# Optimization experiments

Hardware: AMD Instinct MI355X
Metric: run time of the kernel (lower is better)

## Reference

```python
import jax, jax.numpy as jnp
import numpy as np

N = 30000   # nodes
E = 600000  # edges (avg degree 20)
H = 128     # hidden_channels
L = 4       # num_layers
G = 64      # graphs in batch


def _init(key, shape, fan_in):
    return (jax.random.normal(key, shape, jnp.float32) / np.sqrt(fan_in)).astype(jnp.float32)


def setup_inputs() -> dict:
    key = jax.random.key(0)
    ks = jax.random.split(key, 24)
    x = jax.random.normal(ks[0], (N, 1), jnp.float32)
    pos = jax.random.normal(ks[1], (N, 3), jnp.float32)
    edge_index = jax.random.randint(ks[2], (2, E), 0, N, dtype=jnp.int32).astype(jnp.int64)
    batch = jnp.sort(jax.random.randint(ks[3], (N,), 0, G, dtype=jnp.int32)).astype(jnp.int64)

    emb_w = _init(ks[4], (1, H), 1)
    emb_b = jnp.zeros((H,), jnp.float32)

    # stacked per-layer params: msg MLP (2H+1 -> H -> H), node MLP (2H -> H -> H)
    msg_w1 = _init(ks[5], (L, 2 * H + 1, H), 2 * H + 1)
    msg_b1 = jnp.zeros((L, H), jnp.float32)
    msg_w2 = _init(ks[6], (L, H, H), H)
    msg_b2 = jnp.zeros((L, H), jnp.float32)
    node_w1 = _init(ks[7], (L, 2 * H, H), 2 * H)
    node_b1 = jnp.zeros((L, H), jnp.float32)
    node_w2 = _init(ks[8], (L, H, H), H)
    node_b2 = jnp.zeros((L, H), jnp.float32)

    out_w1 = _init(ks[9], (H, 32), H)
    out_b1 = jnp.zeros((32,), jnp.float32)
    out_w2 = _init(ks[10], (32, 1), 32)
    out_b2 = jnp.zeros((1,), jnp.float32)

    return {
        "x": x, "pos": pos, "edge_index": edge_index, "batch": batch,
        "emb_w": emb_w, "emb_b": emb_b,
        "msg_w1": msg_w1, "msg_b1": msg_b1, "msg_w2": msg_w2, "msg_b2": msg_b2,
        "node_w1": node_w1, "node_b1": node_b1, "node_w2": node_w2, "node_b2": node_b2,
        "out_w1": out_w1, "out_b1": out_b1, "out_w2": out_w2, "out_b2": out_b2,
    }


def reference(x, pos, edge_index, batch,
              emb_w, emb_b,
              msg_w1, msg_b1, msg_w2, msg_b2,
              node_w1, node_b1, node_w2, node_b2,
              out_w1, out_b1, out_w2, out_b2):
    row, col = edge_index[0], edge_index[1]  # row = source j, col = target i
    # edge scalar: squared distance (computed once, reused across layers)
    dist_sq = jnp.sum((pos[row] - pos[col]) ** 2, axis=-1, keepdims=True)  # [E,1]

    h = x @ emb_w + emb_b  # [N,H]
    for l in range(L):
        x_j = h[row]   # source features
        x_i = h[col]   # target features
        m = jnp.concatenate([x_i, x_j, dist_sq], axis=-1)           # [E, 2H+1]
        m = jax.nn.silu(m @ msg_w1[l] + msg_b1[l]) @ msg_w2[l] + msg_b2[l]  # [E,H]
        aggr = jax.ops.segment_sum(m, col, num_segments=N)          # scatter-add to targets
        nh = jnp.concatenate([h, aggr], axis=-1)                    # [N, 2H]
        h = jax.nn.silu(nh @ node_w1[l] + node_b1[l]) @ node_w2[l] + node_b2[l]
        # dropout omitted for deterministic reference (eval mode)

    g = jax.ops.segment_sum(h, batch, num_segments=G)               # global_add_pool [G,H]
    return jax.nn.silu(g @ out_w1 + out_b1) @ out_w2 + out_b2       # [G,1]
```

## Files before the change

### kernel.cpp

```cpp
#include <hip/hip_runtime.h>

typedef unsigned short u16;
typedef __bf16 bf16x8 __attribute__((ext_vector_type(8)));
typedef float f32x4 __attribute__((ext_vector_type(4)));

#define HN 128
#define TM 64
#define LTM 32
#define ASTRIDE 136

__device__ __forceinline__ u16 f2bf(float f) {
  union { float f; unsigned u; } v; v.f = f;
  unsigned r = v.u + 0x7fffu + ((v.u >> 16) & 1u);
  return (u16)(r >> 16);
}
__device__ __forceinline__ float bf2f(u16 v) {
  union { unsigned u; float f; } x; x.u = ((unsigned)v) << 16; return x.f;
}
__device__ __forceinline__ float bflo(unsigned v) {
  union { unsigned u; float f; } x; x.u = v << 16; return x.f;
}
__device__ __forceinline__ float bfhi(unsigned v) {
  union { unsigned u; float f; } x; x.u = v & 0xffff0000u; return x.f;
}
__device__ __forceinline__ float silu_f(float x) {
  float e = __builtin_amdgcn_exp2f(-1.442695041f * x);
  return x * __builtin_amdgcn_rcpf(1.f + e);
}

__global__ void pack_weights(const float* __restrict__ msg_w1, const float* __restrict__ msg_w2,
                             const float* __restrict__ node_w1, const float* __restrict__ node_w2,
                             u16* __restrict__ pw, int* __restrict__ deg,
                             float* __restrict__ g, int N_, int GH) {
  int id = blockIdx.x * 256 + threadIdx.x;
  if (id < N_) deg[id] = 0;
  if (id < GH) g[id] = 0.f;
  if (id >= 4 * 6 * 16384) return;
  int l = id / (6 * 16384);
  int rem = id % (6 * 16384);
  int m = rem / 16384;
  int e = rem % 16384;
  int kg = e >> 10;
  int n = (e >> 3) & 127;
  int j = e & 7;
  int k = kg * 8 + j;
  float v = 0.f;
  switch (m) {
    case 0: v = msg_w1[(l * 257 + k) * 128 + n]; break;
    case 1: v = msg_w1[(l * 257 + 128 + k) * 128 + n]; break;
    case 2: v = msg_w2[(l * 128 + k) * 128 + n]; break;
    case 3: v = node_w1[(l * 256 + k) * 128 + n]; break;
    case 4: v = node_w1[(l * 256 + 128 + k) * 128 + n]; break;
    case 5: v = node_w2[(l * 128 + k) * 128 + n]; break;
  }
  pw[id] = f2bf(v);
}

__device__ __forceinline__ void gemm64(const u16* s_A, const u16* s_W,
                                       int w, int quad, int m16, f32x4 acc[8]) {
#pragma unroll
  for (int ks = 0; ks < 4; ks++) {
    bf16x8 a = *(const bf16x8*)&s_A[(w * 16 + m16) * ASTRIDE + ks * 32 + quad * 8];
#pragma unroll
    for (int ct = 0; ct < 8; ct++) {
      bf16x8 b = *(const bf16x8*)&s_W[(ks * 4 + quad) * 1024 + (ct * 16 + m16) * 8];
      acc[ct] = __builtin_amdgcn_mfma_f32_16x16x32_bf16(a, b, acc[ct], 0, 0, 0);
    }
  }
}

__device__ __forceinline__ void gemm32_gb(const u16* s_A, const u16* __restrict__ gW,
                                          int rh, int ch, int quad, int m16, f32x4 acc[4]) {
#pragma unroll
  for (int ks = 0; ks < 4; ks++) {
    bf16x8 a = *(const bf16x8*)&s_A[(rh * 16 + m16) * ASTRIDE + ks * 32 + quad * 8];
#pragma unroll
    for (int ct = 0; ct < 4; ct++) {
      bf16x8 b = *(const bf16x8*)&gW[(ks * 4 + quad) * 1024 + ((ch * 4 + ct) * 16 + m16) * 8];
      acc[ct] = __builtin_amdgcn_mfma_f32_16x16x32_bf16(a, b, acc[ct], 0, 0, 0);
    }
  }
}

__device__ __forceinline__ void gemm32_ra_gb(const bf16x8 aH[4], const u16* __restrict__ gW,
                                             int ch, int quad, int m16, f32x4 acc[4]) {
#pragma unroll
  for (int ks = 0; ks < 4; ks++) {
#pragma unroll
    for (int ct = 0; ct < 4; ct++) {
      bf16x8 b = *(const bf16x8*)&gW[(ks * 4 + quad) * 1024 + ((ch * 4 + ct) * 16 + m16) * 8];
      acc[ct] = __builtin_amdgcn_mfma_f32_16x16x32_bf16(aH[ks], b, acc[ct], 0, 0, 0);
    }
  }
}

__global__ __launch_bounds__(256) void fold_kernel(
    const float* __restrict__ msg_w2, const float* __restrict__ node_w1,
    const float* __restrict__ msg_b2, const u16* __restrict__ pw,
    u16* __restrict__ pwc, float* __restrict__ vc) {
  __shared__ __align__(16) u16 s_A[TM * ASTRIDE];
  __shared__ __align__(16) u16 s_W[16384];
  const int t = threadIdx.x;
  const int w = t >> 6, lane = t & 63, quad = lane >> 4, m16 = lane & 15;
  const int b = blockIdx.x, l = b >> 1, half = b & 1;
  const int tile0 = half * 64;

  {
    int r = t >> 2, qo = (t & 3) * 32;
    const float4* src = (const float4*)(msg_w2 + (size_t)(l * 128 + tile0 + r) * 128 + qo);
    u16* dst = s_A + r * ASTRIDE + qo;
#pragma unroll
    for (int i = 0; i < 8; i++) {
      float4 v = src[i];
      ushort4 o;
      o.x = f2bf(v.x); o.y = f2bf(v.y); o.z = f2bf(v.z); o.w = f2bf(v.w);
      *(ushort4*)(dst + i * 4) = o;
    }
  }
  {
    const int4* src = (const int4*)(pw + (size_t)(l * 6 + 4) * 16384);
    int4* dst = (int4*)s_W;
#pragma unroll
    for (int i = 0; i < 8; i++) dst[t + i * 256] = src[t + i * 256];
  }
  __syncthreads();
  f32x4 acc[8];
#pragma unroll
  for (int ct = 0; ct < 8; ct++) acc[ct] = {0.f, 0.f, 0.f, 0.f};
  gemm64(s_A, s_W, w, quad, m16, acc);
#pragma unroll
  for (int ct = 0; ct < 8; ct++)
#pragma unroll
    for (int j = 0; j < 4; j++) {
      int k = tile0 + w * 16 + quad * 4 + j;
      int n = ct * 16 + m16;
      pwc[(size_t)l * 16384 + (k >> 3) * 1024 + n * 8 + (k & 7)] = f2bf(acc[ct][j]);
    }
  if (half == 0 && t < 128) {
    float s = 0.f;
    for (int np = 0; np < 128; np++)
      s += msg_b2[l * 128 + np] * node_w1[(size_t)(l * 256 + 128 + np) * 128 + t];
    vc[l * 128 + t] = s;
  }
}

__global__ void hist_kernel(const int* __restrict__ eidx, int* __restrict__ deg,
                            int* __restrict__ rnk, int E_) {
  int e = blockIdx.x * 256 + threadIdx.x;
  if (e < E_) rnk[e] = atomicAdd(&deg[eidx[E_ + e]], 1);
}

__global__ void scan1_kernel(const int* __restrict__ deg, int* __restrict__ off,
                             int* __restrict__ bsum, int n) {
  __shared__ int s[256];
  int t = threadIdx.x;
  int i = blockIdx.x * 256 + t;
  int v = (i < n) ? deg[i] : 0;
  s[t] = v;
  for (int d = 1; d < 256; d <<= 1) {
    __syncthreads();
    int x = (t >= d) ? s[t - d] : 0;
    __syncthreads();
    s[t] += x;
  }
  __syncthreads();
  if (i < n) off[i] = s[t] - v;
  if (t == 255) bsum[blockIdx.x] = s[255];
}

__global__ void scan2_kernel(int* __restrict__ bsum, int nb) {
  __shared__ int s[256];
  int t = threadIdx.x;
  int v = (t < nb) ? bsum[t] : 0;
  s[t] = v;
  for (int d = 1; d < 256; d <<= 1) {
    __syncthreads();
    int x = (t >= d) ? s[t - d] : 0;
    __syncthreads();
    s[t] += x;
  }
  __syncthreads();
  if (t < nb) bsum[t] = s[t] - v;
}

__global__ void scan3_kernel(int* __restrict__ off, const int* __restrict__ bsum, int n) {
  int i = blockIdx.x * 256 + threadIdx.x;
  if (i < n) off[i] += bsum[blockIdx.x];
}

__global__ void scatter_kernel(const int* __restrict__ eidx, const float* __restrict__ pos,
                               const int* __restrict__ off, const int* __restrict__ rnk,
                               int2* __restrict__ es8, int E_) {
  int e = blockIdx.x * 256 + threadIdx.x;
  if (e >= E_) return;
  int sr = eidx[e], tg = eidx[E_ + e];
  float dx = pos[sr * 3 + 0] - pos[tg * 3 + 0];
  float dy = pos[sr * 3 + 1] - pos[tg * 3 + 1];
  float dz = pos[sr * 3 + 2] - pos[tg * 3 + 2];
  float d = dx * dx + dy * dy + dz * dz;
  int p = off[tg] + rnk[e];
  int2 v;
  v.x = sr | (tg << 15);
  v.y = __float_as_int(d);
  es8[p] = v;
}

__global__ __launch_bounds__(256) void proj_kernel(
    const float* __restrict__ x, const float* __restrict__ emb_w,
    const float* __restrict__ emb_b, u16* __restrict__ hbf,
    u16* __restrict__ Pout, u16* __restrict__ Qout,
    const u16* __restrict__ pw, const float* __restrict__ b1, int nnodes) {
  __shared__ __align__(16) u16 s_A[TM * ASTRIDE];
  __shared__ __align__(16) u16 s_W[16384];
  const int t = threadIdx.x;
  const int w = t >> 6, lane = t & 63, quad = lane >> 4, m16 = lane & 15;
  const int tile0 = blockIdx.x * TM;
  {
    int r = t >> 2, qo = (t & 3) * 32;
    int node = tile0 + r;
    if (node >= nnodes) node = nnodes - 1;
    float xv = x[node];
    u16 hv[32];
#pragma unroll
    for (int i = 0; i < 32; i++) hv[i] = f2bf(xv * emb_w[qo + i] + emb_b[qo + i]);
    u16* dst = s_A + r * ASTRIDE + qo;
#pragma unroll
    for (int i = 0; i < 4; i++) *(int4*)(dst + i * 8) = *(int4*)(hv + i * 8);
    u16* gd = hbf + (size_t)node * HN + qo;
#pragma unroll
    for (int i = 0; i < 4; i++) *(int4*)(gd + i * 8) = *(int4*)(hv + i * 8);
  }
  {
    const int4* src = (const int4*)pw;
    int4* dst = (int4*)s_W;
#pragma unroll
    for (int i = 0; i < 8; i++) dst[t + i * 256] = src[t + i * 256];
  }
  __syncthreads();
  f32x4 acc[8];
#pragma unroll
  for (int ct = 0; ct < 8; ct++) acc[ct] = {0.f, 0.f, 0.f, 0.f};
  gemm64(s_A, s_W, w, quad, m16, acc);
  __syncthreads();
  {
    const int4* src = (const int4*)(pw + 16384);
    int4* dst = (int4*)s_W;
#pragma unroll
    for (int i = 0; i < 8; i++) dst[t + i * 256] = src[t + i * 256];
  }
  float bb[8];
#pragma unroll
  for (int ct = 0; ct < 8; ct++) bb[ct] = b1[ct * 16 + m16];
#pragma unroll
  for (int ct = 0; ct < 8; ct++)
#pragma unroll
    for (int j = 0; j < 4; j++) {
      int n = tile0 + w * 16 + quad * 4 + j;
      if (n < nnodes) Pout[(size_t)n * HN + ct * 16 + m16] = f2bf(acc[ct][j] + bb[ct]);
    }
  __syncthreads();
#pragma unroll
  for (int ct = 0; ct < 8; ct++) acc[ct] = {0.f, 0.f, 0.f, 0.f};
  gemm64(s_A, s_W, w, quad, m16, acc);
#pragma unroll
  for (int ct = 0; ct < 8; ct++)
#pragma unroll
    for (int j = 0; j < 4; j++) {
      int n = tile0 + w * 16 + quad * 4 + j;
      if (n < nnodes) Qout[(size_t)n * HN + ct * 16 + m16] = f2bf(acc[ct][j]);
    }
}

__device__ __forceinline__ void edge_step_lds(
    int tg_s, float dd_s, unsigned qv,
    int& cur_s, float& p0, float& p1, float& s0, float& s1,
    const u16* __restrict__ P, float* s_S, int cp,
    float wd0, float wd1, int tile0) {
  if (tg_s != cur_s) {
    if (cur_s >= 0) {
      float* dst = &s_S[(cur_s - tile0) * HN + cp];
      atomicAdd(dst, s0);
      atomicAdd(dst + 1, s1);
    }
    cur_s = tg_s; s0 = 0.f; s1 = 0.f;
    int cg = tg_s < 0 ? 0 : tg_s;
    unsigned pv = *(const unsigned*)&P[(size_t)cg * HN + cp];
    p0 = bflo(pv); p1 = bfhi(pv);
  }
  float x0 = p0 + bflo(qv) + dd_s * wd0;
  float x1 = p1 + bfhi(qv) + dd_s * wd1;
  s0 += silu_f(x0);
  s1 += silu_f(x1);
}

template <bool FUSE>
__global__ __launch_bounds__(256) void layer_kernel(
    const u16* __restrict__ P, const u16* __restrict__ Q,
    const u16* __restrict__ hbf, u16* __restrict__ hout,
    const int* __restrict__ off, const int* __restrict__ deg,
    const float* __restrict__ w1d, const int2* __restrict__ es8,
    const u16* __restrict__ pwc, const float* __restrict__ vc,
    const u16* __restrict__ pwn, const float* __restrict__ b1, const float* __restrict__ b2,
    const u16* __restrict__ pw_next, const float* __restrict__ b1_next,
    u16* __restrict__ Pout, u16* __restrict__ Qout, int nnodes, int E_) {
  __shared__ float s_S[LTM * HN];
  __shared__ __align__(16) u16 s_A[LTM * ASTRIDE];
  const int t = threadIdx.x;
  const int w = t >> 6, lane = t & 63, quad = lane >> 4, m16 = lane & 15;
  const int tile0 = blockIdx.x * LTM;
  const int rh = w >> 1;
  const int ch = w & 1;

  {
    float4 z = {0.f, 0.f, 0.f, 0.f};
    float4* p4 = (float4*)s_S;
#pragma unroll
    for (int i = 0; i < 4; i++) p4[t + i * 256] = z;
  }
  __syncthreads();

  const int cp = lane * 2;
  const float2 wdv = *(const float2*)&w1d[cp];
  const float wd0 = wdv.x, wd1 = wdv.y;
  const int e_lo = off[tile0];
  const int e_hi = (tile0 + LTM < nnodes) ? off[tile0 + LTM] : E_;
  const int span = e_hi - e_lo;
  const int wstart = e_lo + (span * w) / 4;
  const int wend = e_lo + (span * (w + 1)) / 4;
  const int total = wend - wstart;
  const int nchunks = (total + 63) >> 6;

  int cur_s = -1;
  float s0 = 0.f, s1 = 0.f, p0 = 0.f, p1 = 0.f;

  if (nchunks > 0) {
    int2* ebuf = (int2*)(s_A + (w * 8) * ASTRIDE);
    {
      int e = wstart + lane;
      int2 v;
      if (e < wend) v = es8[e];
      else { v.x = (int)0xFFFF8000; v.y = 0; }
      ebuf[lane] = v;
    }
    asm volatile("s_waitcnt lgkmcnt(0)" ::: "memory");
    int tg[8]; float dd[8]; unsigned qv[8];
#pragma unroll
    for (int j = 0; j < 8; j++) {
      int2 v = ebuf[j];
      tg[j] = v.x >> 15; dd[j] = __int_as_float(v.y);
      qv[j] = *(const unsigned*)&Q[(size_t)(v.x & 0x7fff) * HN + cp];
    }

    for (int ci = 0; ci < nchunks; ci++) {
      const int2* cb = ebuf + (ci & 1) * 64;
      const int2* nb = ebuf + ((ci + 1) & 1) * 64;
      int2 vnext; vnext.x = (int)0xFFFF8000; vnext.y = 0;
      {
        int e = wstart + (ci + 1) * 64 + lane;
        if (ci + 1 < nchunks && e < wend) vnext = es8[e];
      }
#pragma unroll
      for (int g = 0; g < 7; g++) {
        int tgn[8]; float ddn[8]; unsigned qvn[8];
#pragma unroll
        for (int j = 0; j < 8; j++) {
          int2 v = cb[(g + 1) * 8 + j];
          tgn[j] = v.x >> 15; ddn[j] = __int_as_float(v.y);
          qvn[j] = *(const unsigned*)&Q[(size_t)(v.x & 0x7fff) * HN + cp];
        }
#pragma unroll
        for (int j = 0; j < 8; j++) {
          int tg_s = __builtin_amdgcn_readfirstlane(tg[j]);
          edge_step_lds(tg_s, dd[j], qv[j], cur_s, p0, p1, s0, s1, P, s_S, cp, wd0, wd1, tile0);
        }
#pragma unroll
        for (int j = 0; j < 8; j++) { tg[j] = tgn[j]; dd[j] = ddn[j]; qv[j] = qvn[j]; }
      }
      ebuf[((ci + 1) & 1) * 64 + lane] = vnext;
      asm volatile("s_waitcnt lgkmcnt(0)" ::: "memory");
      {
        int tgn[8]; float ddn[8]; unsigned qvn[8];
#pragma unroll
        for (int j = 0; j < 8; j++) {
          int2 v = nb[j];
          tgn[j] = v.x >> 15; ddn[j] = __int_as_float(v.y);
          qvn[j] = *(const unsigned*)&Q[(size_t)(v.x & 0x7fff) * HN + cp];
        }
#pragma unroll
        for (int j = 0; j < 8; j++) {
          int tg_s = __builtin_amdgcn_readfirstlane(tg[j]);
          edge_step_lds(tg_s, dd[j], qv[j], cur_s, p0, p1, s0, s1, P, s_S, cp, wd0, wd1, tile0);
        }
#pragma unroll
        for (int j = 0; j < 8; j++) { tg[j] = tgn[j]; dd[j] = ddn[j]; qv[j] = qvn[j]; }
      }
    }
    if (cur_s >= 0) {
      float* dst = &s_S[(cur_s - tile0) * HN + cp];
      atomicAdd(dst, s0);
      atomicAdd(dst + 1, s1);
    }
  }
  __syncthreads();

  {
    int srow = w * 8 + (lane >> 3);
    int scol = (lane & 7) * 16;
    const float4* src = (const float4*)&s_S[srow * HN + scol];
    u16* dst = s_A + srow * ASTRIDE + scol;
#pragma unroll
    for (int i = 0; i < 4; i++) {
      float4 v = src[i];
      ushort4 o;
      o.x = f2bf(v.x); o.y = f2bf(v.y); o.z = f2bf(v.z); o.w = f2bf(v.w);
      *(ushort4*)(dst + i * 4) = o;
    }
  }
  __syncthreads();

  float bb1[4], vcr[4], bb2[4], bbn[4];
#pragma unroll
  for (int ct = 0; ct < 4; ct++) {
    int c = (ch * 4 + ct) * 16 + m16;
    bb1[ct] = b1[c];
    vcr[ct] = vc[c];
    bb2[ct] = b2[c];
    bbn[ct] = FUSE ? b1_next[c] : 0.f;
  }
  int nodem = tile0 + rh * 16 + m16;
  if (nodem >= nnodes) nodem = nnodes - 1;

  f32x4 acc[4];
#pragma unroll
  for (int ct = 0; ct < 4; ct++) acc[ct] = {0.f, 0.f, 0.f, 0.f};
  gemm32_gb(s_A, pwc, rh, ch, quad, m16, acc);

  bf16x8 aH[4];
#pragma unroll
  for (int ks = 0; ks < 4; ks++)
    aH[ks] = *(const bf16x8*)&hbf[(size_t)nodem * HN + ks * 32 + quad * 8];
  gemm32_ra_gb(aH, pwn, ch, quad, m16, acc);

  {
    float degv[4];
#pragma unroll
    for (int j = 0; j < 4; j++) {
      int n = tile0 + rh * 16 + quad * 4 + j;
      if (n >= nnodes) n = nnodes - 1;
      degv[j] = (float)deg[n];
    }
#pragma unroll
    for (int ct = 0; ct < 4; ct++)
#pragma unroll
      for (int j = 0; j < 4; j++) {
        int row = rh * 16 + quad * 4 + j;
        float xv = acc[ct][j] + bb1[ct] + degv[j] * vcr[ct];
        s_A[row * ASTRIDE + (ch * 4 + ct) * 16 + m16] = f2bf(silu_f(xv));
      }
  }
  __syncthreads();

#pragma unroll
  for (int ct = 0; ct < 4; ct++) acc[ct] = {0.f, 0.f, 0.f, 0.f};
  gemm32_gb(s_A, pwn + 32768, rh, ch, quad, m16, acc);

#pragma unroll
  for (int ct = 0; ct < 4; ct++)
#pragma unroll
    for (int j = 0; j < 4; j++) {
      int row = rh * 16 + quad * 4 + j;
      int n = tile0 + row;
      u16 hv = f2bf(acc[ct][j] + bb2[ct]);
      if (n < nnodes) hout[(size_t)n * HN + (ch * 4 + ct) * 16 + m16] = hv;
      if (FUSE) s_A[row * ASTRIDE + (ch * 4 + ct) * 16 + m16] = hv;
    }

  if (FUSE) {
    __syncthreads();
#pragma unroll
    for (int ct = 0; ct < 4; ct++) acc[ct] = {0.f, 0.f, 0.f, 0.f};
    gemm32_gb(s_A, pw_next, rh, ch, quad, m16, acc);
#pragma unroll
    for (int ct = 0; ct < 4; ct++)
#pragma unroll
      for (int j = 0; j < 4; j++) {
        int n = tile0 + rh * 16 + quad * 4 + j;
        if (n < nnodes) Pout[(size_t)n * HN + (ch * 4 + ct) * 16 + m16] = f2bf(acc[ct][j] + bbn[ct]);
      }
#pragma unroll
    for (int ct = 0; ct < 4; ct++) acc[ct] = {0.f, 0.f, 0.f, 0.f};
    gemm32_gb(s_A, pw_next + 16384, rh, ch, quad, m16, acc);
#pragma unroll
    for (int ct = 0; ct < 4; ct++)
#pragma unroll
      for (int j = 0; j < 4; j++) {
        int n = tile0 + rh * 16 + quad * 4 + j;
        if (n < nnodes) Qout[(size_t)n * HN + (ch * 4 + ct) * 16 + m16] = f2bf(acc[ct][j]);
      }
  }
}

__global__ __launch_bounds__(256) void pool_kernel(
    const u16* __restrict__ h, const int* __restrict__ batch,
    float* __restrict__ g, int N) {
  __shared__ int s_b[64];
  const int t = threadIdx.x;
  const int n0 = blockIdx.x * 64;
  if (t < 64) {
    int n = n0 + t;
    s_b[t] = (n < N) ? batch[n] : -1;
  }
  __syncthreads();
  const int cp = (t & 63) * 2;
  const int rg = t >> 6;
  int cur = -1;
  float s0 = 0.f, s1 = 0.f;
#pragma unroll 4
  for (int i = 0; i < 16; i++) {
    int r = rg * 16 + i;
    int b = s_b[r];
    if (b < 0) break;
    if (b != cur) {
      if (cur >= 0) {
        atomicAdd(&g[cur * HN + cp], s0);
        atomicAdd(&g[cur * HN + cp + 1], s1);
      }
      cur = b; s0 = 0.f; s1 = 0.f;
    }
    unsigned v = *(const unsigned*)&h[(size_t)(n0 + r) * HN + cp];
    s0 += bf2f((u16)(v & 0xffffu));
    s1 += bf2f((u16)(v >> 16));
  }
  if (cur >= 0) {
    atomicAdd(&g[cur * HN + cp], s0);
    atomicAdd(&g[cur * HN + cp + 1], s1);
  }
}

__global__ __launch_bounds__(64) void out_kernel(
    const float* __restrict__ g, const float* __restrict__ w1,
    const float* __restrict__ b1, const float* __restrict__ w2,
    const float* __restrict__ b2, float* __restrict__ out) {
  const int gi = blockIdx.x;
  const int t = threadIdx.x;
  const int c = t & 31, kh = t >> 5;
  float s = 0.f;
  for (int k = kh * 64; k < kh * 64 + 64; k++)
    s += g[gi * HN + k] * w1[k * 32 + c];
  s += __shfl_down(s, 32);
  float r = 0.f;
  if (kh == 0) r = silu_f(s + b1[c]) * w2[c];
  r += __shfl_down(r, 16);
  r += __shfl_down(r, 8);
  r += __shfl_down(r, 4);
  r += __shfl_down(r, 2);
  r += __shfl_down(r, 1);
  if (t == 0) out[gi] = r + b2[0];
}

extern "C" void kernel_launch(void* const* d_in, const int* in_sizes, int n_in,
                              void* d_out, int out_size, void* d_ws, size_t ws_size,
                              hipStream_t stream) {
  const float* x = (const float*)d_in[0];
  const float* pos = (const float*)d_in[1];
  const int* eidx = (const int*)d_in[2];
  const int* batch = (const int*)d_in[3];
  const float* emb_w = (const float*)d_in[4];
  const float* emb_b = (const float*)d_in[5];
  const float* msg_w1 = (const float*)d_in[6];
  const float* msg_b1 = (const float*)d_in[7];
  const float* msg_w2 = (const float*)d_in[8];
  const float* msg_b2 = (const float*)d_in[9];
  const float* node_w1 = (const float*)d_in[10];
  const float* node_b1 = (const float*)d_in[11];
  const float* node_w2 = (const float*)d_in[12];
  const float* node_b2 = (const float*)d_in[13];
  const float* out_w1 = (const float*)d_in[14];
  const float* out_b1 = (const float*)d_in[15];
  const float* out_w2 = (const float*)d_in[16];
  const float* out_b2 = (const float*)d_in[17];
  float* outp = (float*)d_out;

  const int N = 30000, E = 600000, G = 64;
  const size_t NH = (size_t)N * HN;

  u16* hA = (u16*)d_ws;
  u16* hB = hA + NH;
  u16* Pa = hB + NH;
  u16* Qa = Pa + NH;
  u16* Pb = Qa + NH;
  u16* Qb = Pb + NH;
  int2* es8 = (int2*)(Qb + NH);
  int* deg = (int*)(es8 + E);
  int* off = deg + N;
  int* bsum = off + N;
  float* g = (float*)(bsum + 128);
  u16* pw = (u16*)(g + G * HN);
  u16* pwc = pw + (size_t)4 * 6 * 16384;
  float* vcb = (float*)(pwc + (size_t)4 * 16384);
  int* rnk = (int*)Pb;

  const int NB = (N + 255) / 256;
  const int NTB = (N + TM - 1) / TM;
  const int NLB = (N + LTM - 1) / LTM;

  pack_weights<<<(4 * 6 * 16384 + 255) / 256, 256, 0, stream>>>(
      msg_w1, msg_w2, node_w1, node_w2, pw, deg, g, N, G * HN);
  fold_kernel<<<8, 256, 0, stream>>>(msg_w2, node_w1, msg_b2, pw, pwc, vcb);

  hist_kernel<<<(E + 255) / 256, 256, 0, stream>>>(eidx, deg, rnk, E);
  scan1_kernel<<<NB, 256, 0, stream>>>(deg, off, bsum, N);
  scan2_kernel<<<1, 256, 0, stream>>>(bsum, NB);
  scan3_kernel<<<NB, 256, 0, stream>>>(off, bsum, N);
  scatter_kernel<<<(E + 255) / 256, 256, 0, stream>>>(eidx, pos, off, rnk, es8, E);

  proj_kernel<<<NTB, 256, 0, stream>>>(x, emb_w, emb_b, hA, Pa, Qa, pw, msg_b1, N);

  u16* hcur = hA;
  u16* hnext = hB;
  u16* Pin = Pa; u16* Qin = Qa;
  u16* Pot = Pb; u16* Qot = Qb;
  for (int l = 0; l < 4; l++) {
    const u16* pwl = pw + (size_t)(l * 6) * 16384;
    const float* w1d = msg_w1 + (size_t)(l * 257 + 256) * 128;
    if (l < 3) {
      const u16* pw_next = pw + (size_t)((l + 1) * 6) * 16384;
      layer_kernel<true><<<NLB, 256, 0, stream>>>(
          Pin, Qin, hcur, hnext, off, deg, w1d, es8,
          pwc + (size_t)l * 16384, vcb + l * 128,
          pwl + 3 * 16384, node_b1 + l * 128, node_b2 + l * 128,
          pw_next, msg_b1 + (l + 1) * 128, Pot, Qot, N, E);
    } else {
      layer_kernel<false><<<NLB, 256, 0, stream>>>(
          Pin, Qin, hcur, hnext, off, deg, w1d, es8,
          pwc + (size_t)l * 16384, vcb + l * 128,
          pwl + 3 * 16384, node_b1 + l * 128, node_b2 + l * 128,
          nullptr, nullptr, nullptr, nullptr, N, E);
    }
    u16* tmp = hcur; hcur = hnext; hnext = tmp;
    tmp = Pin; Pin = Pot; Pot = tmp;
    tmp = Qin; Qin = Qot; Qot = tmp;
  }

  pool_kernel<<<(N + 63) / 64, 256, 0, stream>>>(hcur, batch, g, N);
  out_kernel<<<G, 64, 0, stream>>>(g, out_w1, out_b1, out_w2, out_b2, outp);
}
```

Before: 399.4 us.

## Exploit rank-1 embedding to drop proj kernel and layer-0 gathers

Since h0 = x*emb_w + emb_b is rank-1 in x, the layer-0 message pre-activations become x_i*uP + vP + x_j*uQ, with the u/v vectors precomputed in fold_kernel. The proj_kernel that materialized h0, P and Q for all nodes is removed. Layer 0 now gathers one float of x per edge instead of a bf16 Q row slice, and rebuilds h0 on the fly for the node MLP. This removes one GEMM kernel launch plus large N×H reads and writes. The cost is a third template variant and slightly different rounding, since P and Q are no longer quantized to bf16.

```diff
diff --git a/kernel.cpp b/kernel.cpp
--- a/kernel.cpp
+++ b/kernel.cpp
@@ -97,7 +97,10 @@
 __global__ __launch_bounds__(256) void fold_kernel(
     const float* __restrict__ msg_w2, const float* __restrict__ node_w1,
     const float* __restrict__ msg_b2, const u16* __restrict__ pw,
-    u16* __restrict__ pwc, float* __restrict__ vc) {
+    u16* __restrict__ pwc, float* __restrict__ vc,
+    const float* __restrict__ msg_w1, const float* __restrict__ emb_w,
+    const float* __restrict__ emb_b, const float* __restrict__ msg_b1,
+    float* __restrict__ uv) {
   __shared__ __align__(16) u16 s_A[TM * ASTRIDE];
   __shared__ __align__(16) u16 s_W[16384];
   const int t = threadIdx.x;
@@ -141,6 +144,20 @@
     for (int np = 0; np < 128; np++)
       s += msg_b2[l * 128 + np] * node_w1[(size_t)(l * 256 + 128 + np) * 128 + t];
     vc[l * 128 + t] = s;
+  }
+  if (l == 0 && half == 1 && t < 128) {
+    float up = 0.f, vp = 0.f, uq = 0.f, vq = 0.f;
+    for (int k = 0; k < 128; k++) {
+      float wa = msg_w1[(size_t)k * 128 + t];
+      float wb = msg_w1[(size_t)(128 + k) * 128 + t];
+      up = fmaf(emb_w[k], wa, up);
+      vp = fmaf(emb_b[k], wa, vp);
+      uq = fmaf(emb_w[k], wb, uq);
+      vq = fmaf(emb_b[k], wb, vq);
+    }
+    uv[t] = up;
+    uv[128 + t] = vp + vq + msg_b1[t];
+    uv[256 + t] = uq;
   }
 }
 
@@ -205,72 +222,6 @@
   es8[p] = v;
 }
 
-__global__ __launch_bounds__(256) void proj_kernel(
-    const float* __restrict__ x, const float* __restrict__ emb_w,
-    const float* __restrict__ emb_b, u16* __restrict__ hbf,
-    u16* __restrict__ Pout, u16* __restrict__ Qout,
-    const u16* __restrict__ pw, const float* __restrict__ b1, int nnodes) {
-  __shared__ __align__(16) u16 s_A[TM * ASTRIDE];
-  __shared__ __align__(16) u16 s_W[16384];
-  const int t = threadIdx.x;
-  const int w = t >> 6, lane = t & 63, quad = lane >> 4, m16 = lane & 15;
-  const int tile0 = blockIdx.x * TM;
-  {
-    int r = t >> 2, qo = (t & 3) * 32;
-    int node = tile0 + r;
-    if (node >= nnodes) node = nnodes - 1;
-    float xv = x[node];
-    u16 hv[32];
-#pragma unroll
-    for (int i = 0; i < 32; i++) hv[i] = f2bf(xv * emb_w[qo + i] + emb_b[qo + i]);
-    u16* dst = s_A + r * ASTRIDE + qo;
-#pragma unroll
-    for (int i = 0; i < 4; i++) *(int4*)(dst + i * 8) = *(int4*)(hv + i * 8);
-    u16* gd = hbf + (size_t)node * HN + qo;
-#pragma unroll
-    for (int i = 0; i < 4; i++) *(int4*)(gd + i * 8) = *(int4*)(hv + i * 8);
-  }
-  {
-    const int4* src = (const int4*)pw;
-    int4* dst = (int4*)s_W;
-#pragma unroll
-    for (int i = 0; i < 8; i++) dst[t + i * 256] = src[t + i * 256];
-  }
-  __syncthreads();
-  f32x4 acc[8];
-#pragma unroll
-  for (int ct = 0; ct < 8; ct++) acc[ct] = {0.f, 0.f, 0.f, 0.f};
-  gemm64(s_A, s_W, w, quad, m16, acc);
-  __syncthreads();
-  {
-    const int4* src = (const int4*)(pw + 16384);
-    int4* dst = (int4*)s_W;
-#pragma unroll
-    for (int i = 0; i < 8; i++) dst[t + i * 256] = src[t + i * 256];
-  }
-  float bb[8];
-#pragma unroll
-  for (int ct = 0; ct < 8; ct++) bb[ct] = b1[ct * 16 + m16];
-#pragma unroll
-  for (int ct = 0; ct < 8; ct++)
-#pragma unroll
-    for (int j = 0; j < 4; j++) {
-      int n = tile0 + w * 16 + quad * 4 + j;
-      if (n < nnodes) Pout[(size_t)n * HN + ct * 16 + m16] = f2bf(acc[ct][j] + bb[ct]);
-    }
-  __syncthreads();
-#pragma unroll
-  for (int ct = 0; ct < 8; ct++) acc[ct] = {0.f, 0.f, 0.f, 0.f};
-  gemm64(s_A, s_W, w, quad, m16, acc);
-#pragma unroll
-  for (int ct = 0; ct < 8; ct++)
-#pragma unroll
-    for (int j = 0; j < 4; j++) {
-      int n = tile0 + w * 16 + quad * 4 + j;
-      if (n < nnodes) Qout[(size_t)n * HN + ct * 16 + m16] = f2bf(acc[ct][j]);
-    }
-}
-
 __device__ __forceinline__ void edge_step_lds(
     int tg_s, float dd_s, unsigned qv,
     int& cur_s, float& p0, float& p1, float& s0, float& s1,
@@ -293,7 +244,31 @@
   s1 += silu_f(x1);
 }
 
-template <bool FUSE>
+__device__ __forceinline__ void edge_step_r1(
+    int tg_s, float dd_s, float xs,
+    int& cur_s, float& p0, float& p1, float& s0, float& s1,
+    const float* s_xt, float* s_S, int cp,
+    float wd0, float wd1, float uP0, float uP1, float vP0, float vP1,
+    float uQ0, float uQ1, int tile0) {
+  if (tg_s != cur_s) {
+    if (cur_s >= 0) {
+      float* dst = &s_S[(cur_s - tile0) * HN + cp];
+      atomicAdd(dst, s0);
+      atomicAdd(dst + 1, s1);
+    }
+    cur_s = tg_s; s0 = 0.f; s1 = 0.f;
+    int ci = tg_s < 0 ? 0 : (tg_s - tile0);
+    float xt = s_xt[ci];
+    p0 = fmaf(xt, uP0, vP0);
+    p1 = fmaf(xt, uP1, vP1);
+  }
+  float x0 = fmaf(dd_s, wd0, fmaf(xs, uQ0, p0));
+  float x1 = fmaf(dd_s, wd1, fmaf(xs, uQ1, p1));
+  s0 += silu_f(x0);
+  s1 += silu_f(x1);
+}
+
+template <bool FUSE, bool RANK1>
 __global__ __launch_bounds__(256) void layer_kernel(
     const u16* __restrict__ P, const u16* __restrict__ Q,
     const u16* __restrict__ hbf, u16* __restrict__ hout,
@@ -302,9 +277,13 @@
     const u16* __restrict__ pwc, const float* __restrict__ vc,
     const u16* __restrict__ pwn, const float* __restrict__ b1, const float* __restrict__ b2,
     const u16* __restrict__ pw_next, const float* __restrict__ b1_next,
-    u16* __restrict__ Pout, u16* __restrict__ Qout, int nnodes, int E_) {
+    u16* __restrict__ Pout, u16* __restrict__ Qout,
+    const float* __restrict__ xin, const float* __restrict__ uv,
+    const float* __restrict__ emb_w, const float* __restrict__ emb_b,
+    int nnodes, int E_) {
   __shared__ float s_S[LTM * HN];
   __shared__ __align__(16) u16 s_A[LTM * ASTRIDE];
+  __shared__ float s_xt[LTM];
   const int t = threadIdx.x;
   const int w = t >> 6, lane = t & 63, quad = lane >> 4, m16 = lane & 15;
   const int tile0 = blockIdx.x * LTM;
@@ -316,6 +295,12 @@
     float4* p4 = (float4*)s_S;
 #pragma unroll
     for (int i = 0; i < 4; i++) p4[t + i * 256] = z;
+  }
+  if constexpr (RANK1) {
+    if (t < LTM) {
+      int n = tile0 + t;
+      s_xt[t] = (n < nnodes) ? xin[n] : 0.f;
+    }
   }
   __syncthreads();
 
@@ -333,72 +318,175 @@
   int cur_s = -1;
   float s0 = 0.f, s1 = 0.f, p0 = 0.f, p1 = 0.f;
 
-  if (nchunks > 0) {
-    int2* ebuf = (int2*)(s_A + (w * 8) * ASTRIDE);
-    {
-      int e = wstart + lane;
-      int2 v;
-      if (e < wend) v = es8[e];
-      else { v.x = (int)0xFFFF8000; v.y = 0; }
-      ebuf[lane] = v;
-    }
-    asm volatile("s_waitcnt lgkmcnt(0)" ::: "memory");
-    int tg[8]; float dd[8]; unsigned qv[8];
-#pragma unroll
-    for (int j = 0; j < 8; j++) {
-      int2 v = ebuf[j];
-      tg[j] = v.x >> 15; dd[j] = __int_as_float(v.y);
-      qv[j] = *(const unsigned*)&Q[(size_t)(v.x & 0x7fff) * HN + cp];
-    }
-
-    for (int ci = 0; ci < nchunks; ci++) {
-      const int2* cb = ebuf + (ci & 1) * 64;
-      const int2* nb = ebuf + ((ci + 1) & 1) * 64;
-      int2 vnext; vnext.x = (int)0xFFFF8000; vnext.y = 0;
+  if constexpr (RANK1) {
+    __shared__ float s_xs[4][2][64];
+    const float uP0 = uv[cp], uP1 = uv[cp + 1];
+    const float vP0 = uv[128 + cp], vP1 = uv[128 + cp + 1];
+    const float uQ0 = uv[256 + cp], uQ1 = uv[256 + cp + 1];
+    if (nchunks > 0) {
+      int2* ebuf = (int2*)(s_A + (w * 8) * ASTRIDE);
+      float* xsb = &s_xs[w][0][0];
       {
-        int e = wstart + (ci + 1) * 64 + lane;
-        if (ci + 1 < nchunks && e < wend) vnext = es8[e];
-      }
-#pragma unroll
-      for (int g = 0; g < 7; g++) {
-        int tgn[8]; float ddn[8]; unsigned qvn[8];
-#pragma unroll
-        for (int j = 0; j < 8; j++) {
-          int2 v = cb[(g + 1) * 8 + j];
-          tgn[j] = v.x >> 15; ddn[j] = __int_as_float(v.y);
-          qvn[j] = *(const unsigned*)&Q[(size_t)(v.x & 0x7fff) * HN + cp];
+        int e = wstart + lane;
+        int2 v;
+        if (e < wend) v = es8[e];
+        else { v.x = (int)0xFFFF8000; v.y = 0; }
+        float xl = xin[v.x & 0x7fff];
+        ebuf[lane] = v;
+        xsb[lane] = xl;
+      }
+      asm volatile("s_waitcnt lgkmcnt(0)" ::: "memory");
+      int tg[8]; float dd[8]; float xs[8];
+#pragma unroll
+      for (int j = 0; j < 8; j++) {
+        int2 v = ebuf[j];
+        tg[j] = v.x >> 15; dd[j] = __int_as_float(v.y);
+        xs[j] = xsb[j];
+      }
+
+      for (int ci = 0; ci < nchunks; ci++) {
+        const int cs = (ci & 1), ns = ((ci + 1) & 1);
+        const int2* cb = ebuf + cs * 64;
+        const float* cx = xsb + cs * 64;
+        const int2* nb = ebuf + ns * 64;
+        const float* nx = xsb + ns * 64;
+        int2 vnext; vnext.x = (int)0xFFFF8000; vnext.y = 0;
+        {
+          int e = wstart + (ci + 1) * 64 + lane;
+          if (ci + 1 < nchunks && e < wend) vnext = es8[e];
         }
 #pragma unroll
-        for (int j = 0; j < 8; j++) {
-          int tg_s = __builtin_amdgcn_readfirstlane(tg[j]);
-          edge_step_lds(tg_s, dd[j], qv[j], cur_s, p0, p1, s0, s1, P, s_S, cp, wd0, wd1, tile0);
+        for (int g = 0; g < 3; g++) {
+          int tgn[8]; float ddn[8]; float xsn[8];
+#pragma unroll
+          for (int j = 0; j < 8; j++) {
+            int2 v = cb[(g + 1) * 8 + j];
+            tgn[j] = v.x >> 15; ddn[j] = __int_as_float(v.y);
+            xsn[j] = cx[(g + 1) * 8 + j];
+          }
+#pragma unroll
+          for (int j = 0; j < 8; j++) {
+            int tg_s = __builtin_amdgcn_readfirstlane(tg[j]);
+            edge_step_r1(tg_s, dd[j], xs[j], cur_s, p0, p1, s0, s1, s_xt, s_S, cp,
+                         wd0, wd1, uP0, uP1, vP0, vP1, uQ0, uQ1, tile0);
+          }
+#pragma unroll
+          for (int j = 0; j < 8; j++) { tg[j] = tgn[j]; dd[j] = ddn[j]; xs[j] = xsn[j]; }
         }
-#pragma unroll
-        for (int j = 0; j < 8; j++) { tg[j] = tgn[j]; dd[j] = ddn[j]; qv[j] = qvn[j]; }
-      }
-      ebuf[((ci + 1) & 1) * 64 + lane] = vnext;
+        float xnext = xin[vnext.x & 0x7fff];
+#pragma unroll
+        for (int g = 3; g < 7; g++) {
+          int tgn[8]; float ddn[8]; float xsn[8];
+#pragma unroll
+          for (int j = 0; j < 8; j++) {
+            int2 v = cb[(g + 1) * 8 + j];
+            tgn[j] = v.x >> 15; ddn[j] = __int_as_float(v.y);
+            xsn[j] = cx[(g + 1) * 8 + j];
+          }
+#pragma unroll
+          for (int j = 0; j < 8; j++) {
+            int tg_s = __builtin_amdgcn_readfirstlane(tg[j]);
+            edge_step_r1(tg_s, dd[j], xs[j], cur_s, p0, p1, s0, s1, s_xt, s_S, cp,
+                         wd0, wd1, uP0, uP1, vP0, vP1, uQ0, uQ1, tile0);
+          }
+#pragma unroll
+          for (int j = 0; j < 8; j++) { tg[j] = tgn[j]; dd[j] = ddn[j]; xs[j] = xsn[j]; }
+        }
+        ebuf[ns * 64 + lane] = vnext;
+        xsb[ns * 64 + lane] = xnext;
+        asm volatile("s_waitcnt lgkmcnt(0)" ::: "memory");
+        {
+          int tgn[8]; float ddn[8]; float xsn[8];
+#pragma unroll
+          for (int j = 0; j < 8; j++) {
+            int2 v = nb[j];
+            tgn[j] = v.x >> 15; ddn[j] = __int_as_float(v.y);
+            xsn[j] = nx[j];
+          }
+#pragma unroll
+          for (int j = 0; j < 8; j++) {
+            int tg_s = __builtin_amdgcn_readfirstlane(tg[j]);
+            edge_step_r1(tg_s, dd[j], xs[j], cur_s, p0, p1, s0, s1, s_xt, s_S, cp,
+                         wd0, wd1, uP0, uP1, vP0, vP1, uQ0, uQ1, tile0);
+          }
+#pragma unroll
+          for (int j = 0; j < 8; j++) { tg[j] = tgn[j]; dd[j] = ddn[j]; xs[j] = xsn[j]; }
+        }
+      }
+      if (cur_s >= 0) {
+        float* dst = &s_S[(cur_s - tile0) * HN + cp];
+        atomicAdd(dst, s0);
+        atomicAdd(dst + 1, s1);
+      }
+    }
+  } else {
+    if (nchunks > 0) {
+      int2* ebuf = (int2*)(s_A + (w * 8) * ASTRIDE);
+      {
+        int e = wstart + lane;
+        int2 v;
+        if (e < wend) v = es8[e];
+        else { v.x = (int)0xFFFF8000; v.y = 0; }
+        ebuf[lane] = v;
+      }
       asm volatile("s_waitcnt lgkmcnt(0)" ::: "memory");
-      {
-        int tgn[8]; float ddn[8]; unsigned qvn[8];
-#pragma unroll
-        for (int j = 0; j < 8; j++) {
-          int2 v = nb[j];
-          tgn[j] = v.x >> 15; ddn[j] = __int_as_float(v.y);
-          qvn[j] = *(const unsigned*)&Q[(size_t)(v.x & 0x7fff) * HN + cp];
+      int tg[8]; float dd[8]; unsigned qv[8];
+#pragma unroll
+      for (int j = 0; j < 8; j++) {
+        int2 v = ebuf[j];
+        tg[j] = v.x >> 15; dd[j] = __int_as_float(v.y);
+        qv[j] = *(const unsigned*)&Q[(size_t)(v.x & 0x7fff) * HN + cp];
+      }
+
+      for (int ci = 0; ci < nchunks; ci++) {
+        const int2* cb = ebuf + (ci & 1) * 64;
+        const int2* nb = ebuf + ((ci + 1) & 1) * 64;
+        int2 vnext; vnext.x = (int)0xFFFF8000; vnext.y = 0;
+        {
+          int e = wstart + (ci + 1) * 64 + lane;
+          if (ci + 1 < nchunks && e < wend) vnext = es8[e];
         }
 #pragma unroll
-        for (int j = 0; j < 8; j++) {
-          int tg_s = __builtin_amdgcn_readfirstlane(tg[j]);
-          edge_step_lds(tg_s, dd[j], qv[j], cur_s, p0, p1, s0, s1, P, s_S, cp, wd0, wd1, tile0);
+        for (int g = 0; g < 7; g++) {
+          int tgn[8]; float ddn[8]; unsigned qvn[8];
+#pragma unroll
+          for (int j = 0; j < 8; j++) {
+            int2 v = cb[(g + 1) * 8 + j];
+            tgn[j] = v.x >> 15; ddn[j] = __int_as_float(v.y);
+            qvn[j] = *(const unsigned*)&Q[(size_t)(v.x & 0x7fff) * HN + cp];
+          }
+#pragma unroll
+          for (int j = 0; j < 8; j++) {
+            int tg_s = __builtin_amdgcn_readfirstlane(tg[j]);
+            edge_step_lds(tg_s, dd[j], qv[j], cur_s, p0, p1, s0, s1, P, s_S, cp, wd0, wd1, tile0);
+          }
+#pragma unroll
+          for (int j = 0; j < 8; j++) { tg[j] = tgn[j]; dd[j] = ddn[j]; qv[j] = qvn[j]; }
         }
-#pragma unroll
-        for (int j = 0; j < 8; j++) { tg[j] = tgn[j]; dd[j] = ddn[j]; qv[j] = qvn[j]; }
-      }
-    }
-    if (cur_s >= 0) {
-      float* dst = &s_S[(cur_s - tile0) * HN + cp];
-      atomicAdd(dst, s0);
-      atomicAdd(dst + 1, s1);
+        ebuf[((ci + 1) & 1) * 64 + lane] = vnext;
+        asm volatile("s_waitcnt lgkmcnt(0)" ::: "memory");
+        {
+          int tgn[8]; float ddn[8]; unsigned qvn[8];
+#pragma unroll
+          for (int j = 0; j < 8; j++) {
+            int2 v = nb[j];
+            tgn[j] = v.x >> 15; ddn[j] = __int_as_float(v.y);
+            qvn[j] = *(const unsigned*)&Q[(size_t)(v.x & 0x7fff) * HN + cp];
+          }
+#pragma unroll
+          for (int j = 0; j < 8; j++) {
+            int tg_s = __builtin_amdgcn_readfirstlane(tg[j]);
+            edge_step_lds(tg_s, dd[j], qv[j], cur_s, p0, p1, s0, s1, P, s_S, cp, wd0, wd1, tile0);
+          }
+#pragma unroll
+          for (int j = 0; j < 8; j++) { tg[j] = tgn[j]; dd[j] = ddn[j]; qv[j] = qvn[j]; }
+        }
+      }
+      if (cur_s >= 0) {
+        float* dst = &s_S[(cur_s - tile0) * HN + cp];
+        atomicAdd(dst, s0);
+        atomicAdd(dst + 1, s1);
+      }
     }
   }
   __syncthreads();
@@ -436,9 +524,23 @@
   gemm32_gb(s_A, pwc, rh, ch, quad, m16, acc);
 
   bf16x8 aH[4];
-#pragma unroll
-  for (int ks = 0; ks < 4; ks++)
-    aH[ks] = *(const bf16x8*)&hbf[(size_t)nodem * HN + ks * 32 + quad * 8];
+  if constexpr (RANK1) {
+    float xv = s_xt[rh * 16 + m16];
+#pragma unroll
+    for (int ks = 0; ks < 4; ks++) {
+      u16 hv[8];
+#pragma unroll
+      for (int i = 0; i < 8; i++) {
+        int c = ks * 32 + quad * 8 + i;
+        hv[i] = f2bf(fmaf(xv, emb_w[c], emb_b[c]));
+      }
+      aH[ks] = *(bf16x8*)hv;
+    }
+  } else {
+#pragma unroll
+    for (int ks = 0; ks < 4; ks++)
+      aH[ks] = *(const bf16x8*)&hbf[(size_t)nodem * HN + ks * 32 + quad * 8];
+  }
   gemm32_ra_gb(aH, pwn, ch, quad, m16, acc);
 
   {
@@ -598,15 +700,16 @@
   u16* pw = (u16*)(g + G * HN);
   u16* pwc = pw + (size_t)4 * 6 * 16384;
   float* vcb = (float*)(pwc + (size_t)4 * 16384);
+  float* uvb = vcb + 4 * 128;
   int* rnk = (int*)Pb;
 
   const int NB = (N + 255) / 256;
-  const int NTB = (N + TM - 1) / TM;
   const int NLB = (N + LTM - 1) / LTM;
 
   pack_weights<<<(4 * 6 * 16384 + 255) / 256, 256, 0, stream>>>(
       msg_w1, msg_w2, node_w1, node_w2, pw, deg, g, N, G * HN);
-  fold_kernel<<<8, 256, 0, stream>>>(msg_w2, node_w1, msg_b2, pw, pwc, vcb);
+  fold_kernel<<<8, 256, 0, stream>>>(msg_w2, node_w1, msg_b2, pw, pwc, vcb,
+                                     msg_w1, emb_w, emb_b, msg_b1, uvb);
 
   hist_kernel<<<(E + 255) / 256, 256, 0, stream>>>(eidx, deg, rnk, E);
   scan1_kernel<<<NB, 256, 0, stream>>>(deg, off, bsum, N);
@@ -614,34 +717,40 @@
   scan3_kernel<<<NB, 256, 0, stream>>>(off, bsum, N);
   scatter_kernel<<<(E + 255) / 256, 256, 0, stream>>>(eidx, pos, off, rnk, es8, E);
 
-  proj_kernel<<<NTB, 256, 0, stream>>>(x, emb_w, emb_b, hA, Pa, Qa, pw, msg_b1, N);
-
-  u16* hcur = hA;
-  u16* hnext = hB;
-  u16* Pin = Pa; u16* Qin = Qa;
-  u16* Pot = Pb; u16* Qot = Qb;
+
   for (int l = 0; l < 4; l++) {
     const u16* pwl = pw + (size_t)(l * 6) * 16384;
     const float* w1d = msg_w1 + (size_t)(l * 257 + 256) * 128;
-    if (l < 3) {
-      const u16* pw_next = pw + (size_t)((l + 1) * 6) * 16384;
-      layer_kernel<true><<<NLB, 256, 0, stream>>>(
-          Pin, Qin, hcur, hnext, off, deg, w1d, es8,
+    u16* hin = (l & 1) ? hA : hB;
+    u16* hot = (l & 1) ? hB : hA;
+    u16* Pin = (l & 1) ? Pb : Pa;
+    u16* Qin = (l & 1) ? Qb : Qa;
+    u16* Pot = (l & 1) ? Pa : Pb;
+    u16* Qot = (l & 1) ? Qa : Qb;
+    if (l == 0) {
+      layer_kernel<true, true><<<NLB, 256, 0, stream>>>(
+          Pin, Qin, hin, hot, off, deg, w1d, es8,
           pwc + (size_t)l * 16384, vcb + l * 128,
           pwl + 3 * 16384, node_b1 + l * 128, node_b2 + l * 128,
-          pw_next, msg_b1 + (l + 1) * 128, Pot, Qot, N, E);
-    } else {
-      layer_kernel<false><<<NLB, 256, 0, stream>>>(
-          Pin, Qin, hcur, hnext, off, deg, w1d, es8,
+          pw + (size_t)((l + 1) * 6) * 16384, msg_b1 + (l + 1) * 128, Pot, Qot,
+          x, uvb, emb_w, emb_b, N, E);
+    } else if (l < 3) {
+      layer_kernel<true, false><<<NLB, 256, 0, stream>>>(
+          Pin, Qin, hin, hot, off, deg, w1d, es8,
           pwc + (size_t)l * 16384, vcb + l * 128,
           pwl + 3 * 16384, node_b1 + l * 128, node_b2 + l * 128,
-          nullptr, nullptr, nullptr, nullptr, N, E);
-    }
-    u16* tmp = hcur; hcur = hnext; hnext = tmp;
-    tmp = Pin; Pin = Pot; Pot = tmp;
-    tmp = Qin; Qin = Qot; Qot = tmp;
-  }
-
-  pool_kernel<<<(N + 63) / 64, 256, 0, stream>>>(hcur, batch, g, N);
+          pw + (size_t)((l + 1) * 6) * 16384, msg_b1 + (l + 1) * 128, Pot, Qot,
+          x, uvb, emb_w, emb_b, N, E);
+    } else {
+      layer_kernel<false, false><<<NLB, 256, 0, stream>>>(
+          Pin, Qin, hin, hot, off, deg, w1d, es8,
+          pwc + (size_t)l * 16384, vcb + l * 128,
+          pwl + 3 * 16384, node_b1 + l * 128, node_b2 + l * 128,
+          nullptr, nullptr, nullptr, nullptr,
+          x, uvb, emb_w, emb_b, N, E);
+    }
+  }
+
+  pool_kernel<<<(N + 63) / 64, 256, 0, stream>>>(hB, batch, g, N);
   out_kernel<<<G, 64, 0, stream>>>(g, out_w1, out_b1, out_w2, out_b2, outp);
 }
```

Result: faster. 384.9 us (-3.6%).
